# Kernel tuning notes

Hardware: AMD Instinct MI355X
Metric: run time of the kernel (lower is better)

## Reference

```python
import jax, jax.numpy as jnp
import numpy as np

N_NODES = 100000
N_EDGES = 1600000
F = 64          # node_features (in == out for EvolveGCNO)
HID = 64        # hidden_size


def setup_inputs() -> dict:
    key = jax.random.key(0)
    ks = jax.random.split(key, 12)
    s = 1.0 / np.sqrt(F)
    inp = {
        "x": jax.random.normal(ks[0], (N_NODES, F), dtype=jnp.float32),
        "edge_index": jax.random.randint(ks[1], (2, N_EDGES), 0, N_NODES, dtype=jnp.int64),
        "edge_weight": jax.random.uniform(ks[2], (N_EDGES,), dtype=jnp.float32),
        # evolving GCN weight (initial_weight of EvolveGCNO)
        "W0": jax.random.uniform(ks[3], (F, F), jnp.float32, -s, s),
        # GRU (input_size=F, hidden_size=F): gates ordered r, z, n
        "gru_Wi": jax.random.uniform(ks[4], (3 * F, F), jnp.float32, -s, s),
        "gru_Wh": jax.random.uniform(ks[5], (3 * F, F), jnp.float32, -s, s),
        "gru_bi": jax.random.uniform(ks[6], (3 * F,), jnp.float32, -s, s),
        "gru_bh": jax.random.uniform(ks[7], (3 * F,), jnp.float32, -s, s),
        # projection F -> HID and head HID -> 1
        "proj_W": jax.random.uniform(ks[8], (HID, F), jnp.float32, -s, s),
        "proj_b": jax.random.uniform(ks[9], (HID,), jnp.float32, -s, s),
        "lin_W": jax.random.uniform(ks[10], (1, HID), jnp.float32, -1.0 / np.sqrt(HID), 1.0 / np.sqrt(HID)),
        "lin_b": jax.random.uniform(ks[11], (1,), jnp.float32, -1.0 / np.sqrt(HID), 1.0 / np.sqrt(HID)),
    }
    return inp


def reference(x, edge_index, edge_weight, W0, gru_Wi, gru_Wh, gru_bi, gru_bh,
              proj_W, proj_b, lin_W, lin_b):
    N = x.shape[0]
    # --- EvolveGCNO weight evolution: one GRU step, rows of W0 are both input and hidden ---
    gi = W0 @ gru_Wi.T + gru_bi  # [F, 3F]
    gh = W0 @ gru_Wh.T + gru_bh  # [F, 3F]
    i_r, i_z, i_n = jnp.split(gi, 3, axis=1)
    h_r, h_z, h_n = jnp.split(gh, 3, axis=1)
    r = jax.nn.sigmoid(i_r + h_r)
    z = jax.nn.sigmoid(i_z + h_z)
    n = jnp.tanh(i_n + r * h_n)
    W = (1.0 - z) * n + z * W0  # evolved GCN weight [F, F]

    # --- GCNConv with fixed evolved W: X' = D^-1/2 (A + I) D^-1/2 (X W) ---
    xw = x @ W  # [N, F]
    src, dst = edge_index[0], edge_index[1]
    loop = jnp.arange(N)
    src2 = jnp.concatenate([src, loop])
    dst2 = jnp.concatenate([dst, loop])
    w2 = jnp.concatenate([edge_weight, jnp.ones((N,), xw.dtype)])  # self-loop weight 1
    deg = jax.ops.segment_sum(w2, dst2, num_segments=N)
    dinv = jnp.where(deg > 0, jax.lax.rsqrt(deg), 0.0)
    norm = dinv[src2] * w2 * dinv[dst2]  # [E + N]
    h = jax.ops.segment_sum(xw[src2] * norm[:, None], dst2, num_segments=N)  # [N, F]

    # --- MLP head (dropout is identity in eval) ---
    h = jax.nn.relu(h @ proj_W.T + proj_b)
    return h @ lin_W.T + lin_b  # [N, 1]
```

## Files before the change

### kernel.cpp

```cpp
#include <hip/hip_runtime.h>
#include <stdint.h>

#define FDIM 64
#define BINSH 6
#define NBINS 1563
#define BCAP 1536
#define OVCAP 8192
#define PSTAGE 8192
#define PBLK 196
#define LSTRIDE 72

__device__ __forceinline__ float bf2f(unsigned int u) {
    union { float f; uint32_t i; } v; v.i = (u & 0xFFFFu) << 16; return v.f;
}
__device__ __forceinline__ unsigned short f2bf(float f) {
    union { float f; uint32_t i; } v; v.f = f;
    uint32_t u = v.i;
    u += 0x7FFFu + ((u >> 16) & 1u);
    return (unsigned short)(u >> 16);
}

__global__ __launch_bounds__(256) void k_sentinel(float* out, int N, float val) {
    int n = blockIdx.x * 256 + threadIdx.x;
    if (n < N) out[n] = (n == 0) ? val : 0.f;
}

__global__ __launch_bounds__(1024) void k_prep(
    const int* __restrict__ src, const int* __restrict__ dst,
    const float* __restrict__ ew, int* __restrict__ gcnt,
    int2* __restrict__ part, int* __restrict__ ovf_cnt,
    int* __restrict__ ovs, int* __restrict__ ovd, float* __restrict__ ovw, int E,
    const float* __restrict__ W0, const float* __restrict__ Wi,
    const float* __restrict__ Wh, const float* __restrict__ bi,
    const float* __restrict__ bh, const float* __restrict__ projW,
    float* __restrict__ M) {
    __shared__ char sm[12504];
    int t = threadIdx.x;
    if (blockIdx.x < PBLK) {
        int* hist = (int*)sm;
        int* lcur = hist + NBINS;
        for (int b = t; b < NBINS; b += 1024) hist[b] = 0;
        __syncthreads();
        int e0 = blockIdx.x * PSTAGE;
        int cnt = E - e0; if (cnt > PSTAGE) cnt = PSTAGE;
        for (int i = t; i < cnt; i += 1024) atomicAdd(&hist[dst[e0 + i] >> BINSH], 1);
        __syncthreads();
        for (int b = t; b < NBINS; b += 1024) {
            int h = hist[b];
            lcur[b] = h ? atomicAdd(&gcnt[b], h) : 0;
        }
        __syncthreads();
        for (int i = t; i < cnt; i += 1024) {
            int e = e0 + i;
            int d = dst[e];
            int b = d >> BINSH;
            int p = atomicAdd(&lcur[b], 1);
            if (p < BCAP) {
                part[(size_t)b * BCAP + p] = make_int2(src[e] | ((d & 63) << 20),
                                                       __float_as_int(ew[e]));
            } else {
                int op = atomicAdd(ovf_cnt, 1);
                if (op < OVCAP) {
                    ovs[op] = src[e];
                    ovd[op] = d;
                    ovw[op] = ew[e];
                }
            }
        }
    } else {
        int i = blockIdx.x - PBLK;
        float* w0s  = (float*)sm;
        float* wrow = w0s + 64;
        if (t < 64) w0s[t] = W0[i * 64 + t];
        __syncthreads();
        if (t < 64) {
            int j = t;
            float a0 = 0.f, a1 = 0.f, a2 = 0.f, b0 = 0.f, b1 = 0.f, b2 = 0.f;
#pragma unroll 8
            for (int k = 0; k < 64; k++) {
                float w0k = w0s[k];
                a0 += w0k * Wi[(j)       * 64 + k];
                a1 += w0k * Wi[(64 + j)  * 64 + k];
                a2 += w0k * Wi[(128 + j) * 64 + k];
                b0 += w0k * Wh[(j)       * 64 + k];
                b1 += w0k * Wh[(64 + j)  * 64 + k];
                b2 += w0k * Wh[(128 + j) * 64 + k];
            }
            float ir = a0 + bi[j],        hr = b0 + bh[j];
            float iz = a1 + bi[64 + j],   hz = b1 + bh[64 + j];
            float in_ = a2 + bi[128 + j], hn = b2 + bh[128 + j];
            float r = 1.f / (1.f + expf(-(ir + hr)));
            float z = 1.f / (1.f + expf(-(iz + hz)));
            float n = tanhf(in_ + r * hn);
            wrow[j] = (1.f - z) * n + z * w0s[j];
        }
        __syncthreads();
        if (t < 64) {
            float s = 0.f;
#pragma unroll 8
            for (int q = 0; q < 64; q++) s += wrow[q] * projW[t * 64 + q];
            M[i * 64 + t] = s;
        }
    }
}

__global__ __launch_bounds__(256) void k_xmdeg(
    const float* __restrict__ x, const float* __restrict__ M,
    unsigned short* __restrict__ xm, int N,
    const int* __restrict__ gcnt, const int2* __restrict__ part,
    const int* __restrict__ ovf_cnt, const int* __restrict__ ovd,
    const float* __restrict__ ovw, float* __restrict__ dinv,
    int* __restrict__ loffg) {
    __shared__ char sm[34816];
    int t = threadIdx.x;
    if (blockIdx.x < NBINS) {
        float* xs = (float*)sm;
        float* ms = xs + 64 * 68;
        int nb = blockIdx.x * 64;
#pragma unroll
        for (int i = 0; i < 4; i++) {
            int lin = i * 1024 + t * 4;
            int row = lin >> 6, col = lin & 63;
            int node = nb + row;
            float4 v = make_float4(0.f, 0.f, 0.f, 0.f);
            if (node < N) v = *(const float4*)(x + (size_t)node * 64 + col);
            *(float4*)&xs[row * 68 + col] = v;
            *(float4*)&ms[row * 68 + col] = *(const float4*)(M + lin);
        }
        __syncthreads();
        int tj = t & 15, tn = t >> 4;
        float acc[4][4] = {};
        for (int k = 0; k < 64; k += 4) {
            float4 xv[4], mv[4];
#pragma unroll
            for (int nn = 0; nn < 4; nn++) xv[nn] = *(const float4*)&xs[(tn * 4 + nn) * 68 + k];
#pragma unroll
            for (int kk = 0; kk < 4; kk++) mv[kk] = *(const float4*)&ms[(k + kk) * 68 + tj * 4];
#pragma unroll
            for (int nn = 0; nn < 4; nn++) {
                const float* xp = (const float*)&xv[nn];
#pragma unroll
                for (int kk = 0; kk < 4; kk++) {
                    float xk = xp[kk];
                    const float* mp = (const float*)&mv[kk];
                    acc[nn][0] += xk * mp[0];
                    acc[nn][1] += xk * mp[1];
                    acc[nn][2] += xk * mp[2];
                    acc[nn][3] += xk * mp[3];
                }
            }
        }
#pragma unroll
        for (int nn = 0; nn < 4; nn++) {
            int node = nb + tn * 4 + nn;
            if (node < N) {
                ushort4 o;
                o.x = f2bf(acc[nn][0]); o.y = f2bf(acc[nn][1]);
                o.z = f2bf(acc[nn][2]); o.w = f2bf(acc[nn][3]);
                *(ushort4*)&xm[(size_t)node * 64 + tj * 4] = o;
            }
        }
    } else {
        int b = blockIdx.x - NBINS;
        float* dl   = (float*)sm;
        int*   cntl = (int*)(dl + 64);
        int*   lofl = cntl + 64;
        if (t < 64) { dl[t] = 1.0f; cntl[t] = 0; }
        __syncthreads();
        int c = gcnt[b]; if (c > BCAP) c = BCAP;
        const int2* pe = part + (size_t)b * BCAP;
        for (int i = t; i < c; i += 256) {
            int2 e = pe[i];
            int nl = (e.x >> 20) & 63;
            atomicAdd(&dl[nl], __int_as_float(e.y));
            atomicAdd(&cntl[nl], 1);
        }
        int m = *ovf_cnt; if (m > OVCAP) m = OVCAP;
        for (int i = t; i < m; i += 256) {
            int d = ovd[i];
            if ((d >> BINSH) == b) atomicAdd(&dl[d & 63], ovw[i]);
        }
        __syncthreads();
        if (t == 0) {
            int o = 0;
#pragma unroll 16
            for (int k = 0; k < 64; k++) { lofl[k] = o; o += cntl[k]; }
            lofl[64] = o;
        }
        __syncthreads();
        if (t < 64) {
            int n = b * 64 + t;
            if (n < N) dinv[n] = rsqrtf(dl[t]);
        }
        if (t < 65) loffg[b * LSTRIDE + t] = lofl[t];
    }
}

__global__ __launch_bounds__(256) void k_gf(
    const unsigned short* __restrict__ xm, const float* __restrict__ dinv,
    const int* __restrict__ gcnt, const int2* __restrict__ part,
    const int* __restrict__ loffg,
    const float* __restrict__ projB, const float* __restrict__ linW,
    const float* __restrict__ linB, const int* __restrict__ ovf_cnt,
    const int* __restrict__ ovs, const int* __restrict__ ovd,
    const float* __restrict__ ovw, float* __restrict__ out, int N) {
    __shared__ int  loff[65];
    __shared__ int  lcur[64];
    __shared__ int2 ledge[BCAP];
    __shared__ float pbs[64], lws[64];
    int t = threadIdx.x, b = blockIdx.x;
    if (t < 65) loff[t] = loffg[b * LSTRIDE + t];
    if (t < 64) { pbs[t] = projB[t]; lws[t] = linW[t]; }
    __syncthreads();
    if (t < 64) lcur[t] = loff[t];
    __syncthreads();
    int c = gcnt[b]; if (c > BCAP) c = BCAP;
    const int2* pe = part + (size_t)b * BCAP;
    for (int i = t; i < c; i += 256) {
        int2 e = pe[i];
        int s = e.x & 0xFFFFF;
        float nw = dinv[s] * __int_as_float(e.y);
        int p = atomicAdd(&lcur[(e.x >> 20) & 63], 1);
        ledge[p] = make_int2(e.x, __float_as_int(nw));
    }
    __syncthreads();
    int m = *ovf_cnt; if (m > OVCAP) m = OVCAP;
    float lb = linB[0];
    int wv = t >> 6, lane = t & 63, eg = lane >> 4, fq = lane & 15, f = fq * 4;
    for (int nl = wv; nl < 64; nl += 4) {
        int n = b * 64 + nl;
        if (n >= N) continue;
        float dn = dinv[n];
        int beg = loff[nl], end = loff[nl + 1];
        float ax = 0.f, ay = 0.f, az = 0.f, aw = 0.f;
        float bx = 0.f, by = 0.f, bz = 0.f, bw = 0.f;
        int i = beg + eg;
        for (; i + 4 < end; i += 8) {
            int2 e0 = ledge[i];
            int2 e1 = ledge[i + 4];
            int s0 = e0.x & 0xFFFFF, s1 = e1.x & 0xFFFFF;
            uint2 u0 = *(const uint2*)&xm[(size_t)s0 * 64 + f];
            uint2 u1 = *(const uint2*)&xm[(size_t)s1 * 64 + f];
            float nm0 = __int_as_float(e0.y);
            float nm1 = __int_as_float(e1.y);
            ax += nm0 * bf2f(u0.x);       ay += nm0 * bf2f(u0.x >> 16);
            az += nm0 * bf2f(u0.y);       aw += nm0 * bf2f(u0.y >> 16);
            bx += nm1 * bf2f(u1.x);       by += nm1 * bf2f(u1.x >> 16);
            bz += nm1 * bf2f(u1.y);       bw += nm1 * bf2f(u1.y >> 16);
        }
        for (; i < end; i += 4) {
            int2 e = ledge[i];
            int s = e.x & 0xFFFFF;
            float nm = __int_as_float(e.y);
            uint2 u = *(const uint2*)&xm[(size_t)s * 64 + f];
            ax += nm * bf2f(u.x); ay += nm * bf2f(u.x >> 16);
            az += nm * bf2f(u.y); aw += nm * bf2f(u.y >> 16);
        }
        ax += bx; ay += by; az += bz; aw += bw;
        ax *= dn; ay *= dn; az *= dn; aw *= dn;
        ax += __shfl_xor(ax, 16); ay += __shfl_xor(ay, 16);
        az += __shfl_xor(az, 16); aw += __shfl_xor(aw, 16);
        ax += __shfl_xor(ax, 32); ay += __shfl_xor(ay, 32);
        az += __shfl_xor(az, 32); aw += __shfl_xor(aw, 32);
        if (eg == 0) {
            {
                uint2 u = *(const uint2*)&xm[(size_t)n * 64 + f];
                float sl = dn * dn;
                ax += sl * bf2f(u.x); ay += sl * bf2f(u.x >> 16);
                az += sl * bf2f(u.y); aw += sl * bf2f(u.y >> 16);
            }
            for (int q = 0; q < m; q++) {
                if (ovd[q] == n) {
                    int s = ovs[q];
                    float nm = dinv[s] * ovw[q] * dn;
                    uint2 u = *(const uint2*)&xm[(size_t)s * 64 + f];
                    ax += nm * bf2f(u.x); ay += nm * bf2f(u.x >> 16);
                    az += nm * bf2f(u.y); aw += nm * bf2f(u.y >> 16);
                }
            }
            float v0 = ax + pbs[f],     v1 = ay + pbs[f + 1];
            float v2 = az + pbs[f + 2], v3 = aw + pbs[f + 3];
            float s = (v0 > 0.f ? v0 : 0.f) * lws[f]
                    + (v1 > 0.f ? v1 : 0.f) * lws[f + 1]
                    + (v2 > 0.f ? v2 : 0.f) * lws[f + 2]
                    + (v3 > 0.f ? v3 : 0.f) * lws[f + 3];
            s += __shfl_xor(s, 1); s += __shfl_xor(s, 2);
            s += __shfl_xor(s, 4); s += __shfl_xor(s, 8);
            if (fq == 0) out[n] = s + lb;
        }
    }
}

extern "C" void kernel_launch(void* const* d_in, const int* in_sizes, int n_in,
                              void* d_out, int out_size, void* d_ws, size_t ws_size,
                              hipStream_t stream) {
    const float* x   = (const float*)d_in[0];
    const int*   ei  = (const int*)d_in[1];
    const float* ew  = (const float*)d_in[2];
    const float* W0  = (const float*)d_in[3];
    const float* gWi = (const float*)d_in[4];
    const float* gWh = (const float*)d_in[5];
    const float* gbi = (const float*)d_in[6];
    const float* gbh = (const float*)d_in[7];
    const float* pW  = (const float*)d_in[8];
    const float* pb  = (const float*)d_in[9];
    const float* lW  = (const float*)d_in[10];
    const float* lb  = (const float*)d_in[11];
    float* out = (float*)d_out;

    static const int EXPSZ[12] = {6400000, 3200000, 1600000, 4096, 12288, 12288,
                                  192, 192, 4096, 64, 64, 1};
    int mism = -1;
    for (int i = 0; i < 12 && i < n_in; i++)
        if (in_sizes[i] != EXPSZ[i]) { mism = i; break; }
    if (mism >= 0) {
        k_sentinel<<<(out_size + 255) / 256, 256, 0, stream>>>(out, out_size,
                                                               ldexpf(1.f, 30 + 3 * mism));
        return;
    }

    int N = in_sizes[0] / FDIM;
    int E = in_sizes[1] / 2;
    const int* src = ei;
    const int* dst = ei + E;

    char* wsb = (char*)d_ws;
    float* M       = (float*)(wsb);
    int*   gcnt    = (int*)  (wsb + (32u << 10));
    int*   ovf_cnt = (int*)  (wsb + (39u << 10));
    int*   ovs     = (int*)  (wsb + (44u << 10));
    int*   ovd     = (int*)  (wsb + (76u << 10));
    float* ovw     = (float*)(wsb + (108u << 10));
    float* dinv    = (float*)(wsb + (1u << 20));
    int*   loffg   = (int*)  (wsb + 1572864u);
    int2*  part    = (int2*) (wsb + (2u << 20));
    unsigned short* xm = (unsigned short*)(wsb + (22u << 20));

    hipMemsetAsync(gcnt, 0, (8u << 10), stream);

    k_prep<<<PBLK + 64, 1024, 0, stream>>>(src, dst, ew, gcnt, part,
                                           ovf_cnt, ovs, ovd, ovw, E,
                                           W0, gWi, gWh, gbi, gbh, pW, M);
    k_xmdeg<<<NBINS * 2, 256, 0, stream>>>(x, M, xm, N, gcnt, part,
                                           ovf_cnt, ovd, ovw, dinv, loffg);
    k_gf<<<NBINS, 256, 0, stream>>>(xm, dinv, gcnt, part, loffg, pb, lW, lb,
                                    ovf_cnt, ovs, ovd, ovw, out, N);
}
```

Before: 192.3 us.

## Compute degree via global atomics in prep and prescale xm by dinv

After: 247.2 us. 28.5% more time.

```diff
diff --git a/kernel.cpp b/kernel.cpp
--- a/kernel.cpp
+++ b/kernel.cpp
@@ -8,7 +8,6 @@
 #define OVCAP 8192
 #define PSTAGE 8192
 #define PBLK 196
-#define LSTRIDE 72
 
 __device__ __forceinline__ float bf2f(unsigned int u) {
     union { float f; uint32_t i; } v; v.i = (u & 0xFFFFu) << 16; return v.f;
@@ -29,7 +28,8 @@
     const int* __restrict__ src, const int* __restrict__ dst,
     const float* __restrict__ ew, int* __restrict__ gcnt,
     int2* __restrict__ part, int* __restrict__ ovf_cnt,
-    int* __restrict__ ovs, int* __restrict__ ovd, float* __restrict__ ovw, int E,
+    int* __restrict__ ovs, int* __restrict__ ovd, float* __restrict__ ovw,
+    float* __restrict__ deg, int E,
     const float* __restrict__ W0, const float* __restrict__ Wi,
     const float* __restrict__ Wh, const float* __restrict__ bi,
     const float* __restrict__ bh, const float* __restrict__ projW,
@@ -53,17 +53,19 @@
         for (int i = t; i < cnt; i += 1024) {
             int e = e0 + i;
             int d = dst[e];
+            float w = ew[e];
+            atomicAdd(&deg[d], w);
             int b = d >> BINSH;
             int p = atomicAdd(&lcur[b], 1);
             if (p < BCAP) {
                 part[(size_t)b * BCAP + p] = make_int2(src[e] | ((d & 63) << 20),
-                                                       __float_as_int(ew[e]));
+                                                       __float_as_int(w));
             } else {
                 int op = atomicAdd(ovf_cnt, 1);
                 if (op < OVCAP) {
                     ovs[op] = src[e];
                     ovd[op] = d;
-                    ovw[op] = ew[e];
+                    ovw[op] = w;
                 }
             }
         }
@@ -104,124 +106,107 @@
     }
 }
 
-__global__ __launch_bounds__(256) void k_xmdeg(
+__global__ __launch_bounds__(256) void k_xm(
     const float* __restrict__ x, const float* __restrict__ M,
     unsigned short* __restrict__ xm, int N,
-    const int* __restrict__ gcnt, const int2* __restrict__ part,
-    const int* __restrict__ ovf_cnt, const int* __restrict__ ovd,
-    const float* __restrict__ ovw, float* __restrict__ dinv,
-    int* __restrict__ loffg) {
+    const float* __restrict__ deg, float* __restrict__ dinv) {
     __shared__ char sm[34816];
     int t = threadIdx.x;
-    if (blockIdx.x < NBINS) {
-        float* xs = (float*)sm;
-        float* ms = xs + 64 * 68;
-        int nb = blockIdx.x * 64;
-#pragma unroll
-        for (int i = 0; i < 4; i++) {
-            int lin = i * 1024 + t * 4;
-            int row = lin >> 6, col = lin & 63;
-            int node = nb + row;
-            float4 v = make_float4(0.f, 0.f, 0.f, 0.f);
-            if (node < N) v = *(const float4*)(x + (size_t)node * 64 + col);
-            *(float4*)&xs[row * 68 + col] = v;
-            *(float4*)&ms[row * 68 + col] = *(const float4*)(M + lin);
-        }
-        __syncthreads();
-        int tj = t & 15, tn = t >> 4;
-        float acc[4][4] = {};
-        for (int k = 0; k < 64; k += 4) {
-            float4 xv[4], mv[4];
-#pragma unroll
-            for (int nn = 0; nn < 4; nn++) xv[nn] = *(const float4*)&xs[(tn * 4 + nn) * 68 + k];
-#pragma unroll
-            for (int kk = 0; kk < 4; kk++) mv[kk] = *(const float4*)&ms[(k + kk) * 68 + tj * 4];
-#pragma unroll
-            for (int nn = 0; nn < 4; nn++) {
-                const float* xp = (const float*)&xv[nn];
-#pragma unroll
-                for (int kk = 0; kk < 4; kk++) {
-                    float xk = xp[kk];
-                    const float* mp = (const float*)&mv[kk];
-                    acc[nn][0] += xk * mp[0];
-                    acc[nn][1] += xk * mp[1];
-                    acc[nn][2] += xk * mp[2];
-                    acc[nn][3] += xk * mp[3];
-                }
-            }
-        }
+    float* xs = (float*)sm;
+    float* ms = xs + 64 * 68;
+    int nb = blockIdx.x * 64;
+#pragma unroll
+    for (int i = 0; i < 4; i++) {
+        int lin = i * 1024 + t * 4;
+        int row = lin >> 6, col = lin & 63;
+        int node = nb + row;
+        float4 v = make_float4(0.f, 0.f, 0.f, 0.f);
+        if (node < N) v = *(const float4*)(x + (size_t)node * 64 + col);
+        *(float4*)&xs[row * 68 + col] = v;
+        *(float4*)&ms[row * 68 + col] = *(const float4*)(M + lin);
+    }
+    __syncthreads();
+    int tj = t & 15, tn = t >> 4;
+    float acc[4][4] = {};
+    for (int k = 0; k < 64; k += 4) {
+        float4 xv[4], mv[4];
+#pragma unroll
+        for (int nn = 0; nn < 4; nn++) xv[nn] = *(const float4*)&xs[(tn * 4 + nn) * 68 + k];
+#pragma unroll
+        for (int kk = 0; kk < 4; kk++) mv[kk] = *(const float4*)&ms[(k + kk) * 68 + tj * 4];
 #pragma unroll
         for (int nn = 0; nn < 4; nn++) {
-            int node = nb + tn * 4 + nn;
-            if (node < N) {
-                ushort4 o;
-                o.x = f2bf(acc[nn][0]); o.y = f2bf(acc[nn][1]);
-                o.z = f2bf(acc[nn][2]); o.w = f2bf(acc[nn][3]);
-                *(ushort4*)&xm[(size_t)node * 64 + tj * 4] = o;
-            }
-        }
-    } else {
-        int b = blockIdx.x - NBINS;
-        float* dl   = (float*)sm;
-        int*   cntl = (int*)(dl + 64);
-        int*   lofl = cntl + 64;
-        if (t < 64) { dl[t] = 1.0f; cntl[t] = 0; }
-        __syncthreads();
-        int c = gcnt[b]; if (c > BCAP) c = BCAP;
-        const int2* pe = part + (size_t)b * BCAP;
-        for (int i = t; i < c; i += 256) {
-            int2 e = pe[i];
-            int nl = (e.x >> 20) & 63;
-            atomicAdd(&dl[nl], __int_as_float(e.y));
-            atomicAdd(&cntl[nl], 1);
-        }
-        int m = *ovf_cnt; if (m > OVCAP) m = OVCAP;
-        for (int i = t; i < m; i += 256) {
-            int d = ovd[i];
-            if ((d >> BINSH) == b) atomicAdd(&dl[d & 63], ovw[i]);
-        }
-        __syncthreads();
-        if (t == 0) {
-            int o = 0;
-#pragma unroll 16
-            for (int k = 0; k < 64; k++) { lofl[k] = o; o += cntl[k]; }
-            lofl[64] = o;
-        }
-        __syncthreads();
-        if (t < 64) {
-            int n = b * 64 + t;
-            if (n < N) dinv[n] = rsqrtf(dl[t]);
-        }
-        if (t < 65) loffg[b * LSTRIDE + t] = lofl[t];
+            const float* xp = (const float*)&xv[nn];
+#pragma unroll
+            for (int kk = 0; kk < 4; kk++) {
+                float xk = xp[kk];
+                const float* mp = (const float*)&mv[kk];
+                acc[nn][0] += xk * mp[0];
+                acc[nn][1] += xk * mp[1];
+                acc[nn][2] += xk * mp[2];
+                acc[nn][3] += xk * mp[3];
+            }
+        }
+    }
+#pragma unroll
+    for (int nn = 0; nn < 4; nn++) {
+        int node = nb + tn * 4 + nn;
+        if (node < N) {
+            float dr = rsqrtf(deg[node] + 1.0f);
+            ushort4 o;
+            o.x = f2bf(acc[nn][0] * dr); o.y = f2bf(acc[nn][1] * dr);
+            o.z = f2bf(acc[nn][2] * dr); o.w = f2bf(acc[nn][3] * dr);
+            *(ushort4*)&xm[(size_t)node * 64 + tj * 4] = o;
+            if (tj == 0) dinv[node] = dr;
+        }
     }
 }
 
 __global__ __launch_bounds__(256) void k_gf(
     const unsigned short* __restrict__ xm, const float* __restrict__ dinv,
     const int* __restrict__ gcnt, const int2* __restrict__ part,
-    const int* __restrict__ loffg,
     const float* __restrict__ projB, const float* __restrict__ linW,
     const float* __restrict__ linB, const int* __restrict__ ovf_cnt,
     const int* __restrict__ ovs, const int* __restrict__ ovd,
     const float* __restrict__ ovw, float* __restrict__ out, int N) {
     __shared__ int  loff[65];
     __shared__ int  lcur[64];
+    __shared__ int  cntl[64];
     __shared__ int2 ledge[BCAP];
     __shared__ float pbs[64], lws[64];
     int t = threadIdx.x, b = blockIdx.x;
-    if (t < 65) loff[t] = loffg[b * LSTRIDE + t];
-    if (t < 64) { pbs[t] = projB[t]; lws[t] = linW[t]; }
-    __syncthreads();
-    if (t < 64) lcur[t] = loff[t];
+    if (t < 64) { pbs[t] = projB[t]; lws[t] = linW[t]; cntl[t] = 0; }
     __syncthreads();
     int c = gcnt[b]; if (c > BCAP) c = BCAP;
     const int2* pe = part + (size_t)b * BCAP;
-    for (int i = t; i < c; i += 256) {
-        int2 e = pe[i];
-        int s = e.x & 0xFFFFF;
-        float nw = dinv[s] * __int_as_float(e.y);
-        int p = atomicAdd(&lcur[(e.x >> 20) & 63], 1);
-        ledge[p] = make_int2(e.x, __float_as_int(nw));
+    int2 er[6];
+#pragma unroll
+    for (int k = 0; k < 6; k++) {
+        int i = t + (k << 8);
+        if (i < c) {
+            int2 e = pe[i];
+            er[k] = e;
+            atomicAdd(&cntl[(e.x >> 20) & 63], 1);
+        }
+    }
+    __syncthreads();
+    if (t == 0) {
+        int o = 0;
+#pragma unroll 16
+        for (int k = 0; k < 64; k++) { loff[k] = o; o += cntl[k]; }
+        loff[64] = o;
+    }
+    __syncthreads();
+    if (t < 64) lcur[t] = loff[t];
+    __syncthreads();
+#pragma unroll
+    for (int k = 0; k < 6; k++) {
+        int i = t + (k << 8);
+        if (i < c) {
+            int2 e = er[k];
+            int p = atomicAdd(&lcur[(e.x >> 20) & 63], 1);
+            ledge[p] = e;
+        }
     }
     __syncthreads();
     int m = *ovf_cnt; if (m > OVCAP) m = OVCAP;
@@ -232,54 +217,76 @@
         if (n >= N) continue;
         float dn = dinv[n];
         int beg = loff[nl], end = loff[nl + 1];
-        float ax = 0.f, ay = 0.f, az = 0.f, aw = 0.f;
-        float bx = 0.f, by = 0.f, bz = 0.f, bw = 0.f;
+        float a0 = 0.f, a1 = 0.f, a2 = 0.f, a3 = 0.f;
+        float b0 = 0.f, b1 = 0.f, b2 = 0.f, b3 = 0.f;
+        float c0 = 0.f, c1 = 0.f, c2 = 0.f, c3 = 0.f;
+        float d0 = 0.f, d1 = 0.f, d2 = 0.f, d3 = 0.f;
         int i = beg + eg;
+        for (; i + 12 < end; i += 16) {
+            int2 e0 = ledge[i];
+            int2 e1 = ledge[i + 4];
+            int2 e2 = ledge[i + 8];
+            int2 e3 = ledge[i + 12];
+            uint2 u0 = *(const uint2*)&xm[(size_t)(e0.x & 0xFFFFF) * 64 + f];
+            uint2 u1 = *(const uint2*)&xm[(size_t)(e1.x & 0xFFFFF) * 64 + f];
+            uint2 u2 = *(const uint2*)&xm[(size_t)(e2.x & 0xFFFFF) * 64 + f];
+            uint2 u3 = *(const uint2*)&xm[(size_t)(e3.x & 0xFFFFF) * 64 + f];
+            float w0 = __int_as_float(e0.y);
+            float w1 = __int_as_float(e1.y);
+            float w2 = __int_as_float(e2.y);
+            float w3 = __int_as_float(e3.y);
+            a0 += w0 * bf2f(u0.x); a1 += w0 * bf2f(u0.x >> 16);
+            a2 += w0 * bf2f(u0.y); a3 += w0 * bf2f(u0.y >> 16);
+            b0 += w1 * bf2f(u1.x); b1 += w1 * bf2f(u1.x >> 16);
+            b2 += w1 * bf2f(u1.y); b3 += w1 * bf2f(u1.y >> 16);
+            c0 += w2 * bf2f(u2.x); c1 += w2 * bf2f(u2.x >> 16);
+            c2 += w2 * bf2f(u2.y); c3 += w2 * bf2f(u2.y >> 16);
+            d0 += w3 * bf2f(u3.x); d1 += w3 * bf2f(u3.x >> 16);
+            d2 += w3 * bf2f(u3.y); d3 += w3 * bf2f(u3.y >> 16);
+        }
         for (; i + 4 < end; i += 8) {
             int2 e0 = ledge[i];
             int2 e1 = ledge[i + 4];
-            int s0 = e0.x & 0xFFFFF, s1 = e1.x & 0xFFFFF;
-            uint2 u0 = *(const uint2*)&xm[(size_t)s0 * 64 + f];
-            uint2 u1 = *(const uint2*)&xm[(size_t)s1 * 64 + f];
-            float nm0 = __int_as_float(e0.y);
-            float nm1 = __int_as_float(e1.y);
-            ax += nm0 * bf2f(u0.x);       ay += nm0 * bf2f(u0.x >> 16);
-            az += nm0 * bf2f(u0.y);       aw += nm0 * bf2f(u0.y >> 16);
-            bx += nm1 * bf2f(u1.x);       by += nm1 * bf2f(u1.x >> 16);
-            bz += nm1 * bf2f(u1.y);       bw += nm1 * bf2f(u1.y >> 16);
+            uint2 u0 = *(const uint2*)&xm[(size_t)(e0.x & 0xFFFFF) * 64 + f];
+            uint2 u1 = *(const uint2*)&xm[(size_t)(e1.x & 0xFFFFF) * 64 + f];
+            float w0 = __int_as_float(e0.y);
+            float w1 = __int_as_float(e1.y);
+            a0 += w0 * bf2f(u0.x); a1 += w0 * bf2f(u0.x >> 16);
+            a2 += w0 * bf2f(u0.y); a3 += w0 * bf2f(u0.y >> 16);
+            b0 += w1 * bf2f(u1.x); b1 += w1 * bf2f(u1.x >> 16);
+            b2 += w1 * bf2f(u1.y); b3 += w1 * bf2f(u1.y >> 16);
         }
         for (; i < end; i += 4) {
-            int2 e = ledge[i];
-            int s = e.x & 0xFFFFF;
-            float nm = __int_as_float(e.y);
-            uint2 u = *(const uint2*)&xm[(size_t)s * 64 + f];
-            ax += nm * bf2f(u.x); ay += nm * bf2f(u.x >> 16);
-            az += nm * bf2f(u.y); aw += nm * bf2f(u.y >> 16);
-        }
-        ax += bx; ay += by; az += bz; aw += bw;
-        ax *= dn; ay *= dn; az *= dn; aw *= dn;
-        ax += __shfl_xor(ax, 16); ay += __shfl_xor(ay, 16);
-        az += __shfl_xor(az, 16); aw += __shfl_xor(aw, 16);
-        ax += __shfl_xor(ax, 32); ay += __shfl_xor(ay, 32);
-        az += __shfl_xor(az, 32); aw += __shfl_xor(aw, 32);
+            int2 e0 = ledge[i];
+            uint2 u0 = *(const uint2*)&xm[(size_t)(e0.x & 0xFFFFF) * 64 + f];
+            float w0 = __int_as_float(e0.y);
+            a0 += w0 * bf2f(u0.x); a1 += w0 * bf2f(u0.x >> 16);
+            a2 += w0 * bf2f(u0.y); a3 += w0 * bf2f(u0.y >> 16);
+        }
+        a0 += b0 + c0 + d0; a1 += b1 + c1 + d1;
+        a2 += b2 + c2 + d2; a3 += b3 + c3 + d3;
+        a0 *= dn; a1 *= dn; a2 *= dn; a3 *= dn;
+        a0 += __shfl_xor(a0, 16); a1 += __shfl_xor(a1, 16);
+        a2 += __shfl_xor(a2, 16); a3 += __shfl_xor(a3, 16);
+        a0 += __shfl_xor(a0, 32); a1 += __shfl_xor(a1, 32);
+        a2 += __shfl_xor(a2, 32); a3 += __shfl_xor(a3, 32);
         if (eg == 0) {
             {
                 uint2 u = *(const uint2*)&xm[(size_t)n * 64 + f];
-                float sl = dn * dn;
-                ax += sl * bf2f(u.x); ay += sl * bf2f(u.x >> 16);
-                az += sl * bf2f(u.y); aw += sl * bf2f(u.y >> 16);
+                a0 += dn * bf2f(u.x); a1 += dn * bf2f(u.x >> 16);
+                a2 += dn * bf2f(u.y); a3 += dn * bf2f(u.y >> 16);
             }
             for (int q = 0; q < m; q++) {
                 if (ovd[q] == n) {
                     int s = ovs[q];
-                    float nm = dinv[s] * ovw[q] * dn;
+                    float nm = ovw[q] * dn;
                     uint2 u = *(const uint2*)&xm[(size_t)s * 64 + f];
-                    ax += nm * bf2f(u.x); ay += nm * bf2f(u.x >> 16);
-                    az += nm * bf2f(u.y); aw += nm * bf2f(u.y >> 16);
+                    a0 += nm * bf2f(u.x); a1 += nm * bf2f(u.x >> 16);
+                    a2 += nm * bf2f(u.y); a3 += nm * bf2f(u.y >> 16);
                 }
             }
-            float v0 = ax + pbs[f],     v1 = ay + pbs[f + 1];
-            float v2 = az + pbs[f + 2], v3 = aw + pbs[f + 3];
+            float v0 = a0 + pbs[f],     v1 = a1 + pbs[f + 1];
+            float v2 = a2 + pbs[f + 2], v3 = a3 + pbs[f + 3];
             float s = (v0 > 0.f ? v0 : 0.f) * lws[f]
                     + (v1 > 0.f ? v1 : 0.f) * lws[f + 1]
                     + (v2 > 0.f ? v2 : 0.f) * lws[f + 2]
@@ -328,21 +335,20 @@
     float* M       = (float*)(wsb);
     int*   gcnt    = (int*)  (wsb + (32u << 10));
     int*   ovf_cnt = (int*)  (wsb + (39u << 10));
-    int*   ovs     = (int*)  (wsb + (44u << 10));
-    int*   ovd     = (int*)  (wsb + (76u << 10));
-    float* ovw     = (float*)(wsb + (108u << 10));
+    float* deg     = (float*)(wsb + (40u << 10));
+    int*   ovs     = (int*)  (wsb + (448u << 10));
+    int*   ovd     = (int*)  (wsb + (480u << 10));
+    float* ovw     = (float*)(wsb + (512u << 10));
     float* dinv    = (float*)(wsb + (1u << 20));
-    int*   loffg   = (int*)  (wsb + 1572864u);
     int2*  part    = (int2*) (wsb + (2u << 20));
     unsigned short* xm = (unsigned short*)(wsb + (22u << 20));
 
-    hipMemsetAsync(gcnt, 0, (8u << 10), stream);
+    hipMemsetAsync(gcnt, 0, (408u << 10), stream);
 
     k_prep<<<PBLK + 64, 1024, 0, stream>>>(src, dst, ew, gcnt, part,
-                                           ovf_cnt, ovs, ovd, ovw, E,
+                                           ovf_cnt, ovs, ovd, ovw, deg, E,
                                            W0, gWi, gWh, gbi, gbh, pW, M);
-    k_xmdeg<<<NBINS * 2, 256, 0, stream>>>(x, M, xm, N, gcnt, part,
-                                           ovf_cnt, ovd, ovw, dinv, loffg);
-    k_gf<<<NBINS, 256, 0, stream>>>(xm, dinv, gcnt, part, loffg, pb, lW, lb,
+    k_xm<<<NBINS, 256, 0, stream>>>(x, M, xm, N, deg, dinv);
+    k_gf<<<NBINS, 256, 0, stream>>>(xm, dinv, gcnt, part, pb, lW, lb,
                                     ovf_cnt, ovs, ovd, ovw, out, N);
 }
```
